# Kernel optimization log

Measured on AMD Instinct MI355X. Metric: run time of the kernel, lower is better.

## Reference

```python
import jax, jax.numpy as jnp
import numpy as np

NUM_HEADS = 16
EPS = 1e-5


def _ln(x, w, b):
    mu = jnp.mean(x, axis=-1, keepdims=True)
    var = jnp.mean((x - mu) ** 2, axis=-1, keepdims=True)
    return (x - mu) * jax.lax.rsqrt(var + EPS) * w + b


def _ada_ln(x, vol, lw, lb, gamma, beta, vs_w, vs_b):
    y = _ln(x, lw, lb)
    # volatility_scale: Linear(1,1) on vol[..., None] -> sigmoid
    vs = jax.nn.sigmoid(vol[..., None] * vs_w + vs_b)  # (B,S,1)
    return y * (1.0 + vs) * gamma + beta


def setup_inputs() -> dict:
    key = jax.random.key(0)
    ks = jax.random.split(key, 20)
    B, S, H = 8, 1024, 1024
    Hf = 4 * H
    Hg = H // 2
    w = lambda k, i, o: jax.random.normal(k, (i, o), jnp.float32) * 0.02
    inp = {
        'x': jax.random.normal(ks[0], (B, S, H), jnp.float32),
        'volatility': jax.random.uniform(ks[1], (B, S), jnp.float32),
        'Wq': w(ks[2], H, H), 'bq': jnp.zeros((H,), jnp.float32),
        'Wk': w(ks[3], H, H), 'bk': jnp.zeros((H,), jnp.float32),
        'Wv': w(ks[4], H, H), 'bv': jnp.zeros((H,), jnp.float32),
        'Wo': w(ks[5], H, H), 'bo': jnp.zeros((H,), jnp.float32),
        'ln1_w': jnp.ones((H,), jnp.float32), 'ln1_b': jnp.zeros((H,), jnp.float32),
        'gamma1': jnp.ones((), jnp.float32), 'beta1': jnp.zeros((), jnp.float32),
        'vs1_w': jnp.float32(0.3), 'vs1_b': jnp.float32(0.0),
        'ffn_w1': w(ks[6], H, Hf), 'ffn_b1': jnp.zeros((Hf,), jnp.float32),
        'ffn_w2': w(ks[7], Hf, H), 'ffn_b2': jnp.zeros((H,), jnp.float32),
        'gate_w1': w(ks[8], H, Hg), 'gate_b1': jnp.zeros((Hg,), jnp.float32),
        'gate_w2': w(ks[9], Hg, H), 'gate_b2': jnp.zeros((H,), jnp.float32),
        'ln2_w': jnp.ones((H,), jnp.float32), 'ln2_b': jnp.zeros((H,), jnp.float32),
        'gamma2': jnp.ones((), jnp.float32), 'beta2': jnp.zeros((), jnp.float32),
        'vs2_w': jnp.float32(0.3), 'vs2_b': jnp.float32(0.0),
    }
    return inp


def reference(x, volatility, Wq, bq, Wk, bk, Wv, bv, Wo, bo,
              ln1_w, ln1_b, gamma1, beta1, vs1_w, vs1_b,
              ffn_w1, ffn_b1, ffn_w2, ffn_b2,
              gate_w1, gate_b1, gate_w2, gate_b2,
              ln2_w, ln2_b, gamma2, beta2, vs2_w, vs2_b):
    B, S, H = x.shape
    nh = NUM_HEADS
    hd = H // nh
    scale = np.sqrt(hd).astype(np.float32)

    # self-attention (eval mode -> dropout is identity)
    Q = (x @ Wq + bq).reshape(B, S, nh, hd)
    K = (x @ Wk + bk).reshape(B, S, nh, hd)
    V = (x @ Wv + bv).reshape(B, S, nh, hd)
    scores = jnp.einsum('bqhd,bkhd->bhqk', Q, K) / scale
    attn = jax.nn.softmax(scores, axis=-1)
    ctx = jnp.einsum('bhqk,bkhd->bqhd', attn, V).reshape(B, S, H)
    attn_out = ctx @ Wo + bo

    x = x + attn_out
    x = _ada_ln(x, volatility, ln1_w, ln1_b, gamma1, beta1, vs1_w, vs1_b)

    # volatility-adaptive FFN (volatility present -> gated path)
    h = jax.nn.gelu(x @ ffn_w1 + ffn_b1, approximate=False)
    ffn_out = h @ ffn_w2 + ffn_b2
    g = jax.nn.sigmoid(jax.nn.relu(x @ gate_w1 + gate_b1) @ gate_w2 + gate_b2)
    ffn_res = ffn_out * g + x * (1.0 - g)

    x = x + ffn_res
    x = _ada_ln(x, volatility, ln2_w, ln2_b, gamma2, beta2, vs2_w, vs2_b)
    return x
```

## Files before the change

### kernel.cpp

```cpp
#include <hip/hip_runtime.h>
#include <hip/hip_bf16.h>
#include <math.h>


#define HDIM 1024
#define NHEAD 16
#define DHEAD 64
#define NBATCH 8
#define NSEQ 1024
#define NTOK (NBATCH * NSEQ)
#define LNEPS 1e-5f
#define LOG2E_8 0.180336880f

using f32x4 = __attribute__((ext_vector_type(4))) float;
using s16x8 = __attribute__((ext_vector_type(8))) short;
using u16x8 = __attribute__((ext_vector_type(8))) unsigned short;

enum { ACT_NONE = 0, ACT_GELU = 1, ACT_RELU = 2, ACT_SIG = 3 };

__device__ inline float bf2f(unsigned short u) {
    union { unsigned u; float f; } t; t.u = ((unsigned)u) << 16; return t.f;
}
__device__ inline unsigned short f2bf(float f) {
    __hip_bfloat16 h = __float2bfloat16(f);
    return *reinterpret_cast<unsigned short*>(&h);
}
__device__ inline float gelu_f(float t) {
    const float u = t * (0.7978845608f + 0.0356774081f * t * t);
    const float e = __expf(2.f * u);
    const float th = 1.f - 2.f / (e + 1.f);
    return 0.5f * t * (1.f + th);
}

#define GLDS16(g, l) __builtin_amdgcn_global_load_lds( \
    (__attribute__((address_space(1))) void*)(g),      \
    (__attribute__((address_space(3))) void*)(l), 16, 0, 0)

__global__ __launch_bounds__(256)
void cast_bf16_k(const float* __restrict__ in, unsigned short* __restrict__ out, int n4)
{
    for (int i = blockIdx.x * 256 + threadIdx.x; i < n4; i += gridDim.x * 256) {
        float4 v = ((const float4*)in)[i];
        ushort4 o;
        o.x = f2bf(v.x); o.y = f2bf(v.y); o.z = f2bf(v.z); o.w = f2bf(v.w);
        ((ushort4*)out)[i] = o;
    }
}

__global__ __launch_bounds__(256)
void transpose_cast_k(const float* __restrict__ W, unsigned short* __restrict__ Wt,
                      int K, int N)
{
    __shared__ float tile[32][33];
    const int tx = threadIdx.x, ty = threadIdx.y;
    const int k0 = blockIdx.y * 32, n0 = blockIdx.x * 32;
#pragma unroll
    for (int r = 0; r < 32; r += 8)
        tile[ty + r][tx] = W[(size_t)(k0 + ty + r) * N + n0 + tx];
    __syncthreads();
#pragma unroll
    for (int r = 0; r < 32; r += 8)
        Wt[(size_t)(n0 + ty + r) * K + k0 + tx] = f2bf(tile[tx][ty + r]);
}

__global__ __launch_bounds__(256)
void transpose_v_k(const unsigned short* __restrict__ vb, unsigned short* __restrict__ vtb)
{
    __shared__ unsigned short t[64][72];
    const int tid = threadIdx.x;
    const int b = blockIdx.z, h = blockIdx.y;
    const int s0 = blockIdx.x * 64;
    {
        const int r = tid >> 3, c = (tid & 7) * 8;
        *(u16x8*)&t[r][c] =
            *(const u16x8*)&vb[((size_t)(b * NSEQ + s0 + r)) * HDIM + h * DHEAD + c];
        *(u16x8*)&t[r + 32][c] =
            *(const u16x8*)&vb[((size_t)(b * NSEQ + s0 + r + 32)) * HDIM + h * DHEAD + c];
    }
    __syncthreads();
    {
        const int d = tid & 63, sc = (tid >> 6) * 16;
        u16x8 o0, o1;
#pragma unroll
        for (int i = 0; i < 8; ++i) o0[i] = t[sc + i][d];
#pragma unroll
        for (int i = 0; i < 8; ++i) o1[i] = t[sc + 8 + i][d];
        unsigned short* dst = &vtb[((size_t)((b * NHEAD + h) * DHEAD + d)) * NSEQ + s0 + sc];
        *(u16x8*)dst = o0;
        *(u16x8*)(dst + 8) = o1;
    }
}

template<int BN, int ACT, bool HAS_ADD, bool OUT_BF>
__global__ __launch_bounds__(512, 2)
void gemm8_k(const unsigned short* __restrict__ A, const unsigned short* __restrict__ Bt,
             const float* __restrict__ bias, const float* __restrict__ add,
             void* __restrict__ Cv, int M, int N, int K)
{
    extern __shared__ __align__(16) unsigned short lds[];
    constexpr int BM = 256, BK = 64;
    constexpr int WN = (BN == 256) ? 4 : 2;
    constexpr int WM = 8 / WN;
    constexpr int MREP = BM / (WM * 16);
    constexpr int NREP = BN / (WN * 16);
    constexpr int ASZ = BM * BK;
    constexpr int BSZ = BN * BK;
    constexpr int AR = 4;
    constexpr int BR = (BN == 256) ? 4 : 2;
    constexpr int NSPLIT = (BN == 256) ? 2 : 1;
    constexpr int NPH = 2 * NSPLIT;
    constexpr int MI_PER = MREP / 2;
    constexpr int NJ_PER = NREP / NSPLIT;

    const int tid = threadIdx.x;
    const int lane = tid & 63;
    const int w = tid >> 6;
    const int wr = w / WN;
    const int wc = w % WN;
    const int m0 = blockIdx.y * BM;
    const int n0 = blockIdx.x * BN;
    const int fr = lane & 15;
    const int fo = lane >> 4;

    const int srow = tid >> 3;
    const int sslot = (tid & 7) ^ (srow & 7);
    const size_t a_base = (size_t)(m0 + srow) * K + sslot * 8;
    const size_t b_base = (size_t)(n0 + srow) * K + sslot * 8;

    f32x4 acc[MREP][NREP] = {};

    auto stage = [&](int t) {
        const int buf = t & 1;
        unsigned short* ad = lds + buf * ASZ + w * 512;
        unsigned short* bd = lds + 2 * ASZ + buf * BSZ + w * 512;
        const unsigned short* as_ = A + a_base + (size_t)t * BK;
        const unsigned short* bs_ = Bt + b_base + (size_t)t * BK;
#pragma unroll
        for (int j = 0; j < AR; ++j)
            GLDS16(as_ + (size_t)j * 64 * K, ad + j * 4096);
#pragma unroll
        for (int j = 0; j < BR; ++j)
            GLDS16(bs_ + (size_t)j * 64 * K, bd + j * 4096);
    };

    const int NT = K / BK;
    stage(0);

    for (int t = 0; t < NT; ++t) {
        if (t + 1 < NT) {
            stage(t + 1);
            if constexpr (BN == 256) asm volatile("s_waitcnt vmcnt(8)" ::: "memory");
            else                     asm volatile("s_waitcnt vmcnt(6)" ::: "memory");
        } else {
            asm volatile("s_waitcnt vmcnt(0)" ::: "memory");
        }
        __builtin_amdgcn_s_barrier();

        const char* Ab = (const char*)(lds + (t & 1) * ASZ);
        const char* Bb = (const char*)(lds + 2 * ASZ + (t & 1) * BSZ);

#pragma unroll
        for (int ph = 0; ph < NPH; ++ph) {
            const int mh = ph / NSPLIT, nh = ph % NSPLIT;
            s16x8 af[MI_PER][2], bfr[NJ_PER][2];
#pragma unroll
            for (int i = 0; i < MI_PER; ++i) {
                const int row = wr * (BM / WM) + (mh * MI_PER + i) * 16 + fr;
                const int sw = (row & 7) << 4;
#pragma unroll
                for (int kk = 0; kk < 2; ++kk)
                    af[i][kk] = *(const s16x8*)(Ab + row * 128 + ((kk * 64 + fo * 16) ^ sw));
            }
#pragma unroll
            for (int j = 0; j < NJ_PER; ++j) {
                const int row = wc * 64 + (nh * NJ_PER + j) * 16 + fr;
                const int sw = (row & 7) << 4;
#pragma unroll
                for (int kk = 0; kk < 2; ++kk)
                    bfr[j][kk] = *(const s16x8*)(Bb + row * 128 + ((kk * 64 + fo * 16) ^ sw));
            }
            __builtin_amdgcn_s_setprio(1);
#pragma unroll
            for (int i = 0; i < MI_PER; ++i)
#pragma unroll
                for (int j = 0; j < NJ_PER; ++j)
#pragma unroll
                    for (int kk = 0; kk < 2; ++kk)
                        acc[mh * MI_PER + i][nh * NJ_PER + j] =
                            __builtin_amdgcn_mfma_f32_16x16x32_bf16(
                                af[i][kk], bfr[j][kk],
                                acc[mh * MI_PER + i][nh * NJ_PER + j], 0, 0, 0);
            __builtin_amdgcn_s_setprio(0);
            asm volatile("s_waitcnt lgkmcnt(0)" ::: "memory");
            __builtin_amdgcn_s_barrier();
        }
    }

    float bv[NREP];
#pragma unroll
    for (int j = 0; j < NREP; ++j)
        bv[j] = bias[n0 + wc * 64 + j * 16 + fr];
#pragma unroll
    for (int i = 0; i < MREP; ++i) {
#pragma unroll
        for (int j = 0; j < NREP; ++j) {
            const int gn = n0 + wc * 64 + j * 16 + fr;
#pragma unroll
            for (int r = 0; r < 4; ++r) {
                const int gm = m0 + wr * (BM / WM) + i * 16 + fo * 4 + r;
                float t = acc[i][j][r] + bv[j];
                if (HAS_ADD) t += add[(size_t)gm * N + gn];
                if (ACT == ACT_GELU)      t = gelu_f(t);
                else if (ACT == ACT_RELU) t = fmaxf(t, 0.f);
                else if (ACT == ACT_SIG)  t = 1.f / (1.f + __expf(-t));
                if (OUT_BF) ((unsigned short*)Cv)[(size_t)gm * N + gn] = f2bf(t);
                else        ((float*)Cv)[(size_t)gm * N + gn] = t;
            }
        }
    }
}

__global__ __launch_bounds__(256)
void attn_k(const unsigned short* __restrict__ Qb, const unsigned short* __restrict__ Kb,
            const unsigned short* __restrict__ Vtb, unsigned short* __restrict__ Cb)
{
    __shared__ alignas(16) unsigned short Ks[64 * 64];
    __shared__ alignas(16) unsigned short Vs[64 * 64];
    __shared__ alignas(16) unsigned short Ps[4][16 * 72];

    const int tid = threadIdx.x;
    const int lane = tid & 63;
    const int wid = tid >> 6;
    const int b = blockIdx.z, h = blockIdx.y;
    const int q0 = blockIdx.x * 64 + wid * 16;

    const int kcol = lane & 15;
    const int kofs = (lane >> 4) * 8;
    const size_t qoff = ((size_t)(b * NSEQ + q0 + kcol)) * HDIM + h * DHEAD + kofs;
    const s16x8 qf0 = *(const s16x8*)(Qb + qoff);
    const s16x8 qf1 = *(const s16x8*)(Qb + qoff + 32);

    f32x4 accO[4] = {};
    float mrow[4] = {-1e30f, -1e30f, -1e30f, -1e30f};
    float lrow[4] = {0.f, 0.f, 0.f, 0.f};

    const int lr = lane >> 3;
    const int swz8 = (((lane & 7) ^ lr)) * 8;
    const size_t kbase  = ((size_t)(b * NSEQ)) * HDIM + h * DHEAD;
    const size_t vtbase = ((size_t)((b * NHEAD + h) * DHEAD)) * NSEQ;

    unsigned short* const pw = &Ps[wid][0];
    const int prow = (lane >> 4) * 4;

    for (int kt = 0; kt < NSEQ / 64; ++kt) {
        __syncthreads();
#pragma unroll
        for (int j = 0; j < 2; ++j) {
            const int rowb = wid * 16 + j * 8;
            GLDS16(Kb + kbase + (size_t)(kt * 64 + rowb + lr) * HDIM + swz8,
                   Ks + rowb * 64);
            GLDS16(Vtb + vtbase + (size_t)(rowb + lr) * NSEQ + kt * 64 + swz8,
                   Vs + rowb * 64);
        }
        __syncthreads();

        f32x4 sa[4];
#pragma unroll
        for (int jt = 0; jt < 4; ++jt) {
            const int kr = jt * 16 + kcol;
            const unsigned swz = ((unsigned)(kr & 7)) << 4;
            const s16x8 kf0 = *(const s16x8*)((const char*)Ks + kr * 128 + ((kofs * 2) ^ swz));
            const s16x8 kf1 = *(const s16x8*)((const char*)Ks + kr * 128 + ((64 + kofs * 2) ^ swz));
            f32x4 t = {};
            t = __builtin_amdgcn_mfma_f32_16x16x32_bf16(qf0, kf0, t, 0, 0, 0);
            t = __builtin_amdgcn_mfma_f32_16x16x32_bf16(qf1, kf1, t, 0, 0, 0);
            sa[jt] = t * LOG2E_8;
        }

        float p[4][4];
        float corr[4];
#pragma unroll
        for (int r = 0; r < 4; ++r) {
            float mx = fmaxf(fmaxf(sa[0][r], sa[1][r]), fmaxf(sa[2][r], sa[3][r]));
            mx = fmaxf(mx, __shfl_xor(mx, 1));
            mx = fmaxf(mx, __shfl_xor(mx, 2));
            mx = fmaxf(mx, __shfl_xor(mx, 4));
            mx = fmaxf(mx, __shfl_xor(mx, 8));
            const float mn = fmaxf(mrow[r], mx);
            corr[r] = exp2f(mrow[r] - mn);
            mrow[r] = mn;
            float ps = 0.f;
#pragma unroll
            for (int jt = 0; jt < 4; ++jt) {
                p[jt][r] = exp2f(sa[jt][r] - mn);
                ps += p[jt][r];
            }
            ps += __shfl_xor(ps, 1);
            ps += __shfl_xor(ps, 2);
            ps += __shfl_xor(ps, 4);
            ps += __shfl_xor(ps, 8);
            lrow[r] = lrow[r] * corr[r] + ps;
        }

#pragma unroll
        for (int r = 0; r < 4; ++r)
#pragma unroll
            for (int jt = 0; jt < 4; ++jt)
                pw[(prow + r) * 72 + jt * 16 + kcol] = f2bf(p[jt][r]);

#pragma unroll
        for (int dt = 0; dt < 4; ++dt)
#pragma unroll
            for (int r = 0; r < 4; ++r)
                accO[dt][r] *= corr[r];

#pragma unroll
        for (int kc = 0; kc < 2; ++kc) {
            const s16x8 pa = *(const s16x8*)(pw + kcol * 72 + kc * 32 + kofs);
#pragma unroll
            for (int dt = 0; dt < 4; ++dt) {
                const int dr = dt * 16 + kcol;
                const unsigned swz = ((unsigned)(dr & 7)) << 4;
                const s16x8 vf = *(const s16x8*)((const char*)Vs + dr * 128 +
                                                 ((kc * 64 + kofs * 2) ^ swz));
                accO[dt] = __builtin_amdgcn_mfma_f32_16x16x32_bf16(pa, vf, accO[dt], 0, 0, 0);
            }
        }
    }

    const size_t obase = ((size_t)(b * NSEQ + q0 + prow)) * HDIM + h * DHEAD;
#pragma unroll
    for (int r = 0; r < 4; ++r) {
        const float rl = 1.f / lrow[r];
#pragma unroll
        for (int dt = 0; dt < 4; ++dt)
            Cb[obase + (size_t)r * HDIM + dt * 16 + kcol] = f2bf(accO[dt][r] * rl);
    }
}

template<int MODE, bool WRITE_BF>
__global__ __launch_bounds__(256)
void adaln_k(const float* __restrict__ a, const float* __restrict__ fo,
             const float* __restrict__ g, const float* __restrict__ vol,
             const float* __restrict__ lw, const float* __restrict__ lb,
             const float* __restrict__ gm, const float* __restrict__ bt,
             const float* __restrict__ vsw, const float* __restrict__ vsb,
             float* __restrict__ out, unsigned short* __restrict__ out_bf)
{
    const int tok = blockIdx.x;
    const int tid = threadIdx.x;
    const size_t base = (size_t)tok * HDIM + tid * 4;
    float v[4];
    {
        float4 va = *(const float4*)&a[base];
        if (MODE == 1) {
            float4 vf = *(const float4*)&fo[base];
            float4 vg = *(const float4*)&g[base];
            v[0] = va.x * (2.f - vg.x) + vf.x * vg.x;
            v[1] = va.y * (2.f - vg.y) + vf.y * vg.y;
            v[2] = va.z * (2.f - vg.z) + vf.z * vg.z;
            v[3] = va.w * (2.f - vg.w) + vf.w * vg.w;
        } else {
            v[0] = va.x; v[1] = va.y; v[2] = va.z; v[3] = va.w;
        }
    }
    float sum = v[0] + v[1] + v[2] + v[3];
    float sq  = v[0]*v[0] + v[1]*v[1] + v[2]*v[2] + v[3]*v[3];
#pragma unroll
    for (int off = 32; off > 0; off >>= 1) {
        sum += __shfl_down(sum, off);
        sq  += __shfl_down(sq, off);
    }
    __shared__ float ssum[4], ssq[4];
    const int wid = tid >> 6, lane = tid & 63;
    if (lane == 0) { ssum[wid] = sum; ssq[wid] = sq; }
    __syncthreads();
    const float tsum = ssum[0] + ssum[1] + ssum[2] + ssum[3];
    const float tsq  = ssq[0]  + ssq[1]  + ssq[2]  + ssq[3];
    const float mu   = tsum * (1.f / 1024.f);
    const float var  = tsq * (1.f / 1024.f) - mu * mu;
    const float rstd = rsqrtf(var + LNEPS);
    const float vsv  = 1.f / (1.f + __expf(-(vol[tok] * vsw[0] + vsb[0])));
    const float sca  = (1.f + vsv) * gm[0];
    const float off2 = bt[0];
    const float4 lwv = *(const float4*)&lw[tid * 4];
    const float4 lbv = *(const float4*)&lb[tid * 4];
    float r0 = ((v[0] - mu) * rstd * lwv.x + lbv.x) * sca + off2;
    float r1 = ((v[1] - mu) * rstd * lwv.y + lbv.y) * sca + off2;
    float r2 = ((v[2] - mu) * rstd * lwv.z + lbv.z) * sca + off2;
    float r3 = ((v[3] - mu) * rstd * lwv.w + lbv.w) * sca + off2;
    *(float4*)&out[base] = make_float4(r0, r1, r2, r3);
    if (WRITE_BF) {
        ushort4 ob;
        ob.x = f2bf(r0); ob.y = f2bf(r1); ob.z = f2bf(r2); ob.w = f2bf(r3);
        *(ushort4*)&out_bf[base] = ob;
    }
}

extern "C" void kernel_launch(void* const* d_in, const int* in_sizes, int n_in,
                              void* d_out, int out_size, void* d_ws, size_t ws_size,
                              hipStream_t stream)
{
    (void)in_sizes; (void)n_in; (void)out_size; (void)ws_size;
    const float* x    = (const float*)d_in[0];
    const float* vol  = (const float*)d_in[1];
    const float* Wq   = (const float*)d_in[2];  const float* bq  = (const float*)d_in[3];
    const float* Wk   = (const float*)d_in[4];  const float* bk  = (const float*)d_in[5];
    const float* Wv   = (const float*)d_in[6];  const float* bv  = (const float*)d_in[7];
    const float* Wo   = (const float*)d_in[8];  const float* bo  = (const float*)d_in[9];
    const float* ln1w = (const float*)d_in[10]; const float* ln1b = (const float*)d_in[11];
    const float* gm1  = (const float*)d_in[12]; const float* be1 = (const float*)d_in[13];
    const float* vs1w = (const float*)d_in[14]; const float* vs1b = (const float*)d_in[15];
    const float* fw1  = (const float*)d_in[16]; const float* fb1 = (const float*)d_in[17];
    const float* fw2  = (const float*)d_in[18]; const float* fb2 = (const float*)d_in[19];
    const float* gw1  = (const float*)d_in[20]; const float* gb1 = (const float*)d_in[21];
    const float* gw2  = (const float*)d_in[22]; const float* gb2 = (const float*)d_in[23];
    const float* ln2w = (const float*)d_in[24]; const float* ln2b = (const float*)d_in[25];
    const float* gm2  = (const float*)d_in[26]; const float* be2 = (const float*)d_in[27];
    const float* vs2w = (const float*)d_in[28]; const float* vs2b = (const float*)d_in[29];

    char* w = (char*)d_ws;
    auto MB = [](size_t v) { return v << 20; };
    unsigned short* wtq  = (unsigned short*)(w + MB(0));
    unsigned short* wtk  = (unsigned short*)(w + MB(2));
    unsigned short* wtv  = (unsigned short*)(w + MB(4));
    unsigned short* wto  = (unsigned short*)(w + MB(6));
    unsigned short* wtf1 = (unsigned short*)(w + MB(8));
    unsigned short* wtf2 = (unsigned short*)(w + MB(16));
    unsigned short* wtg1 = (unsigned short*)(w + MB(24));
    unsigned short* wtg2 = (unsigned short*)(w + MB(25));
    unsigned short* xb  = (unsigned short*)(w + MB(26));
    unsigned short* qb  = (unsigned short*)(w + MB(42));
    unsigned short* kb  = (unsigned short*)(w + MB(58));
    unsigned short* vb  = (unsigned short*)(w + MB(74));
    unsigned short* cxb = (unsigned short*)(w + MB(90));
    float*          ao  = (float*)(w + MB(106));
    unsigned short* vtb = (unsigned short*)(w + MB(106));
    float*          x1  = (float*)(w + MB(138));
    unsigned short* x1b = (unsigned short*)(w + MB(170));
    unsigned short* hb  = (unsigned short*)(w + MB(42));
    float*          ffn = (float*)(w + MB(106));
    unsigned short* ghb = (unsigned short*)(w + MB(26));
    float*          gg  = (float*)(w + MB(42));

    dim3 blk(256);
    dim3 tb(32, 8);
    transpose_cast_k<<<dim3(1024/32, 1024/32), tb, 0, stream>>>(Wq, wtq, 1024, 1024);
    transpose_cast_k<<<dim3(1024/32, 1024/32), tb, 0, stream>>>(Wk, wtk, 1024, 1024);
    transpose_cast_k<<<dim3(1024/32, 1024/32), tb, 0, stream>>>(Wv, wtv, 1024, 1024);
    transpose_cast_k<<<dim3(1024/32, 1024/32), tb, 0, stream>>>(Wo, wto, 1024, 1024);
    transpose_cast_k<<<dim3(4096/32, 1024/32), tb, 0, stream>>>(fw1, wtf1, 1024, 4096);
    transpose_cast_k<<<dim3(1024/32, 4096/32), tb, 0, stream>>>(fw2, wtf2, 4096, 1024);
    transpose_cast_k<<<dim3(512/32, 1024/32),  tb, 0, stream>>>(gw1, wtg1, 1024, 512);
    transpose_cast_k<<<dim3(1024/32, 512/32),  tb, 0, stream>>>(gw2, wtg2, 512, 1024);
    cast_bf16_k<<<2048, blk, 0, stream>>>(x, xb, NTOK * HDIM / 4);

    const size_t SH256 = 128 * 1024, SH128 = 96 * 1024;
    gemm8_k<128, ACT_NONE, false, true><<<dim3(8, 32), 512, SH128, stream>>>(
        xb, wtq, bq, nullptr, qb, NTOK, HDIM, HDIM);
    gemm8_k<128, ACT_NONE, false, true><<<dim3(8, 32), 512, SH128, stream>>>(
        xb, wtk, bk, nullptr, kb, NTOK, HDIM, HDIM);
    gemm8_k<128, ACT_NONE, false, true><<<dim3(8, 32), 512, SH128, stream>>>(
        xb, wtv, bv, nullptr, vb, NTOK, HDIM, HDIM);
    transpose_v_k<<<dim3(NSEQ / 64, NHEAD, NBATCH), blk, 0, stream>>>(vb, vtb);
    attn_k<<<dim3(NSEQ / 64, NHEAD, NBATCH), blk, 0, stream>>>(qb, kb, vtb, cxb);
    gemm8_k<128, ACT_NONE, true, false><<<dim3(8, 32), 512, SH128, stream>>>(
        cxb, wto, bo, x, ao, NTOK, HDIM, HDIM);
    adaln_k<0, true><<<dim3(NTOK), blk, 0, stream>>>(
        ao, nullptr, nullptr, vol, ln1w, ln1b, gm1, be1, vs1w, vs1b, x1, x1b);
    gemm8_k<256, ACT_GELU, false, true><<<dim3(16, 32), 512, SH256, stream>>>(
        x1b, wtf1, fb1, nullptr, hb, NTOK, 4096, HDIM);
    gemm8_k<128, ACT_NONE, false, false><<<dim3(8, 32), 512, SH128, stream>>>(
        hb, wtf2, fb2, nullptr, ffn, NTOK, HDIM, 4096);
    gemm8_k<128, ACT_RELU, false, true><<<dim3(4, 32), 512, SH128, stream>>>(
        x1b, wtg1, gb1, nullptr, ghb, NTOK, 512, HDIM);
    gemm8_k<128, ACT_SIG, false, false><<<dim3(8, 32), 512, SH128, stream>>>(
        ghb, wtg2, gb2, nullptr, gg, NTOK, HDIM, 512);
    adaln_k<1, false><<<dim3(NTOK), blk, 0, stream>>>(
        x1, ffn, gg, vol, ln2w, ln2b, gm2, be2, vs2w, vs2b, (float*)d_out, nullptr);
}
```

Baseline: 525.1 us.

## Fuse QKV projection, double-buffer attention, lazy softmax rescale, smaller GEMM tiles

The three Q/K/V projections become one GEMM over a concatenated transposed weight and bias, writing a strided QKV buffer, and the four square weight transposes are merged into one launch. The attention kernel double-buffers its K/V tiles, remaps blocks so each XCD works on a single batch-head, and skips the running-max rescale unless the max grows by more than a threshold. GEMMs gain a BM template parameter and drop to 128x128 tiles with higher occupancy for most calls. The aim is fewer launches, better overlap and more resident blocks, at the cost of extra LDS and a more complex softmax path.

```diff
diff --git a/kernel.cpp b/kernel.cpp
--- a/kernel.cpp
+++ b/kernel.cpp
@@ -9,6 +9,7 @@
 #define NBATCH 8
 #define NSEQ 1024
 #define NTOK (NBATCH * NSEQ)
+#define QKVSTR 3072
 #define LNEPS 1e-5f
 #define LOG2E_8 0.180336880f
 
@@ -48,6 +49,14 @@
 }
 
 __global__ __launch_bounds__(256)
+void concat3_k(const float* __restrict__ a, const float* __restrict__ b,
+               const float* __restrict__ c, float* __restrict__ o)
+{
+    int i = blockIdx.x * 256 + threadIdx.x;
+    o[i] = i < 1024 ? a[i] : (i < 2048 ? b[i - 1024] : c[i - 2048]);
+}
+
+__global__ __launch_bounds__(256)
 void transpose_cast_k(const float* __restrict__ W, unsigned short* __restrict__ Wt,
                       int K, int N)
 {
@@ -61,6 +70,26 @@
 #pragma unroll
     for (int r = 0; r < 32; r += 8)
         Wt[(size_t)(n0 + ty + r) * K + k0 + tx] = f2bf(tile[tx][ty + r]);
+}
+
+__global__ __launch_bounds__(256)
+void transpose_cast4_k(const float* __restrict__ W0, const float* __restrict__ W1,
+                       const float* __restrict__ W2, const float* __restrict__ W3,
+                       unsigned short* __restrict__ Wt)
+{
+    __shared__ float tile[32][33];
+    const int z = blockIdx.z;
+    const float* W = z == 0 ? W0 : z == 1 ? W1 : z == 2 ? W2 : W3;
+    unsigned short* dst = Wt + (size_t)z * HDIM * HDIM;
+    const int tx = threadIdx.x, ty = threadIdx.y;
+    const int k0 = blockIdx.y * 32, n0 = blockIdx.x * 32;
+#pragma unroll
+    for (int r = 0; r < 32; r += 8)
+        tile[ty + r][tx] = W[(size_t)(k0 + ty + r) * HDIM + n0 + tx];
+    __syncthreads();
+#pragma unroll
+    for (int r = 0; r < 32; r += 8)
+        dst[(size_t)(n0 + ty + r) * HDIM + k0 + tx] = f2bf(tile[tx][ty + r]);
 }
 
 __global__ __launch_bounds__(256)
@@ -73,9 +102,9 @@
     {
         const int r = tid >> 3, c = (tid & 7) * 8;
         *(u16x8*)&t[r][c] =
-            *(const u16x8*)&vb[((size_t)(b * NSEQ + s0 + r)) * HDIM + h * DHEAD + c];
+            *(const u16x8*)&vb[((size_t)(b * NSEQ + s0 + r)) * QKVSTR + h * DHEAD + c];
         *(u16x8*)&t[r + 32][c] =
-            *(const u16x8*)&vb[((size_t)(b * NSEQ + s0 + r + 32)) * HDIM + h * DHEAD + c];
+            *(const u16x8*)&vb[((size_t)(b * NSEQ + s0 + r + 32)) * QKVSTR + h * DHEAD + c];
     }
     __syncthreads();
     {
@@ -91,22 +120,23 @@
     }
 }
 
-template<int BN, int ACT, bool HAS_ADD, bool OUT_BF>
-__global__ __launch_bounds__(512, 2)
+template<int BM, int BN, int ACT, bool HAS_ADD, bool OUT_BF>
+__global__ __launch_bounds__(512, (BM == 128) ? 4 : 2)
 void gemm8_k(const unsigned short* __restrict__ A, const unsigned short* __restrict__ Bt,
              const float* __restrict__ bias, const float* __restrict__ add,
              void* __restrict__ Cv, int M, int N, int K)
 {
     extern __shared__ __align__(16) unsigned short lds[];
-    constexpr int BM = 256, BK = 64;
+    constexpr int BK = 64;
     constexpr int WN = (BN == 256) ? 4 : 2;
     constexpr int WM = 8 / WN;
     constexpr int MREP = BM / (WM * 16);
     constexpr int NREP = BN / (WN * 16);
     constexpr int ASZ = BM * BK;
     constexpr int BSZ = BN * BK;
-    constexpr int AR = 4;
-    constexpr int BR = (BN == 256) ? 4 : 2;
+    constexpr int AR = BM / 64;
+    constexpr int BR = BN / 64;
+    constexpr int VM = AR + BR;
     constexpr int NSPLIT = (BN == 256) ? 2 : 1;
     constexpr int NPH = 2 * NSPLIT;
     constexpr int MI_PER = MREP / 2;
@@ -149,8 +179,7 @@
     for (int t = 0; t < NT; ++t) {
         if (t + 1 < NT) {
             stage(t + 1);
-            if constexpr (BN == 256) asm volatile("s_waitcnt vmcnt(8)" ::: "memory");
-            else                     asm volatile("s_waitcnt vmcnt(6)" ::: "memory");
+            asm volatile("s_waitcnt vmcnt(%0)" :: "i"(VM) : "memory");
         } else {
             asm volatile("s_waitcnt vmcnt(0)" ::: "memory");
         }
@@ -221,24 +250,28 @@
 }
 
 __global__ __launch_bounds__(256)
-void attn_k(const unsigned short* __restrict__ Qb, const unsigned short* __restrict__ Kb,
-            const unsigned short* __restrict__ Vtb, unsigned short* __restrict__ Cb)
-{
-    __shared__ alignas(16) unsigned short Ks[64 * 64];
-    __shared__ alignas(16) unsigned short Vs[64 * 64];
+void attn_k(const unsigned short* __restrict__ QKVb, const unsigned short* __restrict__ Vtb,
+            unsigned short* __restrict__ Cb)
+{
+    __shared__ alignas(16) unsigned short Ks[2][64 * 64];
+    __shared__ alignas(16) unsigned short Vs[2][64 * 64];
     __shared__ alignas(16) unsigned short Ps[4][16 * 72];
 
     const int tid = threadIdx.x;
     const int lane = tid & 63;
     const int wid = tid >> 6;
-    const int b = blockIdx.z, h = blockIdx.y;
-    const int q0 = blockIdx.x * 64 + wid * 16;
+    const int L = blockIdx.x;
+    const int xcd = L & 7, slot = L >> 3;
+    const int bh = xcd + ((slot >> 4) << 3);
+    const int qt = slot & 15;
+    const int b = bh >> 4, h = bh & 15;
+    const int q0 = qt * 64 + wid * 16;
 
     const int kcol = lane & 15;
     const int kofs = (lane >> 4) * 8;
-    const size_t qoff = ((size_t)(b * NSEQ + q0 + kcol)) * HDIM + h * DHEAD + kofs;
-    const s16x8 qf0 = *(const s16x8*)(Qb + qoff);
-    const s16x8 qf1 = *(const s16x8*)(Qb + qoff + 32);
+    const size_t qoff = ((size_t)(b * NSEQ + q0 + kcol)) * QKVSTR + h * DHEAD + kofs;
+    const s16x8 qf0 = *(const s16x8*)(QKVb + qoff);
+    const s16x8 qf1 = *(const s16x8*)(QKVb + qoff + 32);
 
     f32x4 accO[4] = {};
     float mrow[4] = {-1e30f, -1e30f, -1e30f, -1e30f};
@@ -246,73 +279,82 @@
 
     const int lr = lane >> 3;
     const int swz8 = (((lane & 7) ^ lr)) * 8;
-    const size_t kbase  = ((size_t)(b * NSEQ)) * HDIM + h * DHEAD;
-    const size_t vtbase = ((size_t)((b * NHEAD + h) * DHEAD)) * NSEQ;
+    const size_t kbase  = ((size_t)(b * NSEQ)) * QKVSTR + HDIM + h * DHEAD;
+    const size_t vtbase = ((size_t)(bh * DHEAD)) * NSEQ;
 
     unsigned short* const pw = &Ps[wid][0];
     const int prow = (lane >> 4) * 4;
 
-    for (int kt = 0; kt < NSEQ / 64; ++kt) {
-        __syncthreads();
+    auto stage = [&](int kt, int buf) {
 #pragma unroll
         for (int j = 0; j < 2; ++j) {
             const int rowb = wid * 16 + j * 8;
-            GLDS16(Kb + kbase + (size_t)(kt * 64 + rowb + lr) * HDIM + swz8,
-                   Ks + rowb * 64);
+            GLDS16(QKVb + kbase + (size_t)(kt * 64 + rowb + lr) * QKVSTR + swz8,
+                   Ks[buf] + rowb * 64);
             GLDS16(Vtb + vtbase + (size_t)(rowb + lr) * NSEQ + kt * 64 + swz8,
-                   Vs + rowb * 64);
-        }
-        __syncthreads();
+                   Vs[buf] + rowb * 64);
+        }
+    };
+
+    stage(0, 0);
+    asm volatile("s_waitcnt vmcnt(0)" ::: "memory");
+    __syncthreads();
+
+    for (int kt = 0; kt < NSEQ / 64; ++kt) {
+        const int cur = kt & 1;
+        if (kt + 1 < NSEQ / 64) stage(kt + 1, cur ^ 1);
 
         f32x4 sa[4];
 #pragma unroll
         for (int jt = 0; jt < 4; ++jt) {
             const int kr = jt * 16 + kcol;
             const unsigned swz = ((unsigned)(kr & 7)) << 4;
-            const s16x8 kf0 = *(const s16x8*)((const char*)Ks + kr * 128 + ((kofs * 2) ^ swz));
-            const s16x8 kf1 = *(const s16x8*)((const char*)Ks + kr * 128 + ((64 + kofs * 2) ^ swz));
+            const s16x8 kf0 = *(const s16x8*)((const char*)Ks[cur] + kr * 128 + ((kofs * 2) ^ swz));
+            const s16x8 kf1 = *(const s16x8*)((const char*)Ks[cur] + kr * 128 + ((64 + kofs * 2) ^ swz));
             f32x4 t = {};
             t = __builtin_amdgcn_mfma_f32_16x16x32_bf16(qf0, kf0, t, 0, 0, 0);
             t = __builtin_amdgcn_mfma_f32_16x16x32_bf16(qf1, kf1, t, 0, 0, 0);
             sa[jt] = t * LOG2E_8;
         }
 
-        float p[4][4];
-        float corr[4];
+        float mx[4];
 #pragma unroll
         for (int r = 0; r < 4; ++r) {
-            float mx = fmaxf(fmaxf(sa[0][r], sa[1][r]), fmaxf(sa[2][r], sa[3][r]));
-            mx = fmaxf(mx, __shfl_xor(mx, 1));
-            mx = fmaxf(mx, __shfl_xor(mx, 2));
-            mx = fmaxf(mx, __shfl_xor(mx, 4));
-            mx = fmaxf(mx, __shfl_xor(mx, 8));
-            const float mn = fmaxf(mrow[r], mx);
-            corr[r] = exp2f(mrow[r] - mn);
-            mrow[r] = mn;
+            float m = fmaxf(fmaxf(sa[0][r], sa[1][r]), fmaxf(sa[2][r], sa[3][r]));
+            m = fmaxf(m, __shfl_xor(m, 1));
+            m = fmaxf(m, __shfl_xor(m, 2));
+            m = fmaxf(m, __shfl_xor(m, 4));
+            m = fmaxf(m, __shfl_xor(m, 8));
+            mx[r] = m;
+        }
+        float dmax = fmaxf(fmaxf(mx[0] - mrow[0], mx[1] - mrow[1]),
+                           fmaxf(mx[2] - mrow[2], mx[3] - mrow[3]));
+        if (!__all(dmax <= 8.f)) {
+#pragma unroll
+            for (int r = 0; r < 4; ++r) {
+                const float mn = fmaxf(mrow[r], mx[r]);
+                const float corr = exp2f(mrow[r] - mn);
+                mrow[r] = mn;
+                lrow[r] *= corr;
+#pragma unroll
+                for (int dt = 0; dt < 4; ++dt) accO[dt][r] *= corr;
+            }
+        }
+#pragma unroll
+        for (int r = 0; r < 4; ++r) {
             float ps = 0.f;
 #pragma unroll
             for (int jt = 0; jt < 4; ++jt) {
-                p[jt][r] = exp2f(sa[jt][r] - mn);
-                ps += p[jt][r];
+                const float p = exp2f(sa[jt][r] - mrow[r]);
+                pw[(prow + r) * 72 + jt * 16 + kcol] = f2bf(p);
+                ps += p;
             }
             ps += __shfl_xor(ps, 1);
             ps += __shfl_xor(ps, 2);
             ps += __shfl_xor(ps, 4);
             ps += __shfl_xor(ps, 8);
-            lrow[r] = lrow[r] * corr[r] + ps;
-        }
-
-#pragma unroll
-        for (int r = 0; r < 4; ++r)
-#pragma unroll
-            for (int jt = 0; jt < 4; ++jt)
-                pw[(prow + r) * 72 + jt * 16 + kcol] = f2bf(p[jt][r]);
-
-#pragma unroll
-        for (int dt = 0; dt < 4; ++dt)
-#pragma unroll
-            for (int r = 0; r < 4; ++r)
-                accO[dt][r] *= corr[r];
+            lrow[r] += ps;
+        }
 
 #pragma unroll
         for (int kc = 0; kc < 2; ++kc) {
@@ -321,11 +363,14 @@
             for (int dt = 0; dt < 4; ++dt) {
                 const int dr = dt * 16 + kcol;
                 const unsigned swz = ((unsigned)(dr & 7)) << 4;
-                const s16x8 vf = *(const s16x8*)((const char*)Vs + dr * 128 +
+                const s16x8 vf = *(const s16x8*)((const char*)Vs[cur] + dr * 128 +
                                                  ((kc * 64 + kofs * 2) ^ swz));
                 accO[dt] = __builtin_amdgcn_mfma_f32_16x16x32_bf16(pa, vf, accO[dt], 0, 0, 0);
             }
         }
+
+        if (kt + 1 < NSEQ / 64) asm volatile("s_waitcnt vmcnt(0)" ::: "memory");
+        __builtin_amdgcn_s_barrier();
     }
 
     const size_t obase = ((size_t)(b * NSEQ + q0 + prow)) * HDIM + h * DHEAD;
@@ -421,60 +466,52 @@
 
     char* w = (char*)d_ws;
     auto MB = [](size_t v) { return v << 20; };
-    unsigned short* wtq  = (unsigned short*)(w + MB(0));
-    unsigned short* wtk  = (unsigned short*)(w + MB(2));
-    unsigned short* wtv  = (unsigned short*)(w + MB(4));
-    unsigned short* wto  = (unsigned short*)(w + MB(6));
-    unsigned short* wtf1 = (unsigned short*)(w + MB(8));
-    unsigned short* wtf2 = (unsigned short*)(w + MB(16));
-    unsigned short* wtg1 = (unsigned short*)(w + MB(24));
-    unsigned short* wtg2 = (unsigned short*)(w + MB(25));
-    unsigned short* xb  = (unsigned short*)(w + MB(26));
-    unsigned short* qb  = (unsigned short*)(w + MB(42));
-    unsigned short* kb  = (unsigned short*)(w + MB(58));
-    unsigned short* vb  = (unsigned short*)(w + MB(74));
-    unsigned short* cxb = (unsigned short*)(w + MB(90));
-    float*          ao  = (float*)(w + MB(106));
-    unsigned short* vtb = (unsigned short*)(w + MB(106));
-    float*          x1  = (float*)(w + MB(138));
-    unsigned short* x1b = (unsigned short*)(w + MB(170));
-    unsigned short* hb  = (unsigned short*)(w + MB(42));
-    float*          ffn = (float*)(w + MB(106));
-    unsigned short* ghb = (unsigned short*)(w + MB(26));
-    float*          gg  = (float*)(w + MB(42));
+    unsigned short* wtqkv = (unsigned short*)(w + MB(0));
+    unsigned short* wto   = (unsigned short*)(w + MB(6));
+    unsigned short* wtf1  = (unsigned short*)(w + MB(8));
+    unsigned short* wtf2  = (unsigned short*)(w + MB(16));
+    unsigned short* wtg1  = (unsigned short*)(w + MB(24));
+    unsigned short* wtg2  = (unsigned short*)(w + MB(25));
+    unsigned short* xb   = (unsigned short*)(w + MB(26));
+    unsigned short* qkvb = (unsigned short*)(w + MB(42));
+    unsigned short* vtb  = (unsigned short*)(w + MB(90));
+    unsigned short* cxb  = (unsigned short*)(w + MB(106));
+    float*          ao   = (float*)(w + MB(122));
+    float*          x1   = (float*)(w + MB(42));
+    unsigned short* x1b  = (unsigned short*)(w + MB(74));
+    unsigned short* hb   = (unsigned short*)(w + MB(90));
+    float*          ffn  = (float*)(w + MB(154));
+    unsigned short* ghb  = (unsigned short*)(w + MB(26));
+    float*          gg   = (float*)(w + MB(90));
+    float*          bqkv = (float*)(w + MB(186));
 
     dim3 blk(256);
     dim3 tb(32, 8);
-    transpose_cast_k<<<dim3(1024/32, 1024/32), tb, 0, stream>>>(Wq, wtq, 1024, 1024);
-    transpose_cast_k<<<dim3(1024/32, 1024/32), tb, 0, stream>>>(Wk, wtk, 1024, 1024);
-    transpose_cast_k<<<dim3(1024/32, 1024/32), tb, 0, stream>>>(Wv, wtv, 1024, 1024);
-    transpose_cast_k<<<dim3(1024/32, 1024/32), tb, 0, stream>>>(Wo, wto, 1024, 1024);
+    transpose_cast4_k<<<dim3(32, 32, 4), tb, 0, stream>>>(Wq, Wk, Wv, Wo, wtqkv);
     transpose_cast_k<<<dim3(4096/32, 1024/32), tb, 0, stream>>>(fw1, wtf1, 1024, 4096);
     transpose_cast_k<<<dim3(1024/32, 4096/32), tb, 0, stream>>>(fw2, wtf2, 4096, 1024);
     transpose_cast_k<<<dim3(512/32, 1024/32),  tb, 0, stream>>>(gw1, wtg1, 1024, 512);
     transpose_cast_k<<<dim3(1024/32, 512/32),  tb, 0, stream>>>(gw2, wtg2, 512, 1024);
     cast_bf16_k<<<2048, blk, 0, stream>>>(x, xb, NTOK * HDIM / 4);
-
-    const size_t SH256 = 128 * 1024, SH128 = 96 * 1024;
-    gemm8_k<128, ACT_NONE, false, true><<<dim3(8, 32), 512, SH128, stream>>>(
-        xb, wtq, bq, nullptr, qb, NTOK, HDIM, HDIM);
-    gemm8_k<128, ACT_NONE, false, true><<<dim3(8, 32), 512, SH128, stream>>>(
-        xb, wtk, bk, nullptr, kb, NTOK, HDIM, HDIM);
-    gemm8_k<128, ACT_NONE, false, true><<<dim3(8, 32), 512, SH128, stream>>>(
-        xb, wtv, bv, nullptr, vb, NTOK, HDIM, HDIM);
-    transpose_v_k<<<dim3(NSEQ / 64, NHEAD, NBATCH), blk, 0, stream>>>(vb, vtb);
-    attn_k<<<dim3(NSEQ / 64, NHEAD, NBATCH), blk, 0, stream>>>(qb, kb, vtb, cxb);
-    gemm8_k<128, ACT_NONE, true, false><<<dim3(8, 32), 512, SH128, stream>>>(
+    concat3_k<<<12, blk, 0, stream>>>(bq, bk, bv, bqkv);
+
+    const size_t SH128 = (128 + 128) * 256;
+    const size_t SH256 = (256 + 256) * 256;
+    gemm8_k<128, 128, ACT_NONE, false, true><<<dim3(24, 64), 512, SH128, stream>>>(
+        xb, wtqkv, bqkv, nullptr, qkvb, NTOK, QKVSTR, HDIM);
+    transpose_v_k<<<dim3(NSEQ / 64, NHEAD, NBATCH), blk, 0, stream>>>(qkvb + 2048, vtb);
+    attn_k<<<dim3(2048), blk, 0, stream>>>(qkvb, vtb, cxb);
+    gemm8_k<128, 128, ACT_NONE, true, false><<<dim3(8, 64), 512, SH128, stream>>>(
         cxb, wto, bo, x, ao, NTOK, HDIM, HDIM);
     adaln_k<0, true><<<dim3(NTOK), blk, 0, stream>>>(
         ao, nullptr, nullptr, vol, ln1w, ln1b, gm1, be1, vs1w, vs1b, x1, x1b);
-    gemm8_k<256, ACT_GELU, false, true><<<dim3(16, 32), 512, SH256, stream>>>(
+    gemm8_k<256, 256, ACT_GELU, false, true><<<dim3(16, 32), 512, SH256, stream>>>(
         x1b, wtf1, fb1, nullptr, hb, NTOK, 4096, HDIM);
-    gemm8_k<128, ACT_NONE, false, false><<<dim3(8, 32), 512, SH128, stream>>>(
+    gemm8_k<128, 128, ACT_NONE, false, false><<<dim3(8, 64), 512, SH128, stream>>>(
         hb, wtf2, fb2, nullptr, ffn, NTOK, HDIM, 4096);
-    gemm8_k<128, ACT_RELU, false, true><<<dim3(4, 32), 512, SH128, stream>>>(
+    gemm8_k<128, 128, ACT_RELU, false, true><<<dim3(4, 64), 512, SH128, stream>>>(
         x1b, wtg1, gb1, nullptr, ghb, NTOK, 512, HDIM);
-    gemm8_k<128, ACT_SIG, false, false><<<dim3(8, 32), 512, SH128, stream>>>(
+    gemm8_k<128, 128, ACT_SIG, false, false><<<dim3(8, 64), 512, SH128, stream>>>(
         ghb, wtg2, gb2, nullptr, gg, NTOK, HDIM, 512);
     adaln_k<1, false><<<dim3(NTOK), blk, 0, stream>>>(
         x1, ffn, gg, vol, ln2w, ln2b, gm2, be2, vs2w, vs2b, (float*)d_out, nullptr);
```

Measured after the change: 519.0 us. About the same (-1.1%).
